# Kernel optimization log

Hardware: AMD Instinct MI355X
Metric: run time of the kernel (lower is better)

Reference implementation:

```python
import jax, jax.numpy as jnp
import numpy as np

# Orbital structure for basis {A: [2s, 2p, 1d]} -> full_basis l values
LS = [0, 0, 1, 1, 2]
DIMS = [2 * l + 1 for l in LS]            # [1,1,3,3,5]
OFFS = np.concatenate([[0], np.cumsum(DIMS)]).astype(int)
NORB = int(sum(DIMS))                      # 13

# Upper-triangular orbital-pair layout of the flat feature vector
PAIRS = []
_off = 0
for _i in range(len(LS)):
    for _j in range(_i, len(LS)):
        PAIRS.append((_i, _j, _off))
        _off += DIMS[_i] * DIMS[_j]
FEAT_DIM = _off                            # 107

N_ATOMS, N_EDGES, N_KPTS = 256, 4096, 4


def _assemble_blocks(feat):
    """[B, FEAT_DIM] -> [B, NORB, NORB], upper-tri orbital blocks, 0.5 on diagonal pairs."""
    B = feat.shape[0]
    blk = jnp.zeros((B, NORB, NORB), feat.dtype)
    for (i, j, o) in PAIRS:
        di, dj = DIMS[i], DIMS[j]
        f = 0.5 if i == j else 1.0
        blk = blk.at[:, OFFS[i]:OFFS[i] + di, OFFS[j]:OFFS[j] + dj].set(
            f * feat[:, o:o + di * dj].reshape(B, di, dj))
    return blk


def setup_inputs() -> dict:
    key = jax.random.key(0)
    k1, k2, k3, k4, k5 = jax.random.split(key, 5)
    return {
        "orbpair_hopping": jax.random.normal(k1, (N_EDGES, FEAT_DIM), jnp.float32),
        "orbpair_onsite": jax.random.normal(k2, (N_ATOMS, FEAT_DIM), jnp.float32),
        "kpoints": jax.random.uniform(k3, (N_KPTS, 3), jnp.float32),
        "edge_cell_shift": jax.random.randint(k4, (N_EDGES, 3), -3, 4).astype(jnp.float32),
        "edge_index": jax.random.randint(k5, (2, N_EDGES), 0, N_ATOMS),
    }


def reference(orbpair_hopping, orbpair_onsite, kpoints, edge_cell_shift, edge_index):
    hop = _assemble_blocks(orbpair_hopping)      # [E, norb, norb]
    onsite = _assemble_blocks(orbpair_onsite)    # [N, norb, norb]
    N, K = onsite.shape[0], kpoints.shape[0]
    cplx = jnp.complex64

    # phase[k, e] = exp(-i 2pi k . R_e)
    phase = jnp.exp(-2j * jnp.pi * (kpoints @ edge_cell_shift.T)).astype(cplx)  # [K, E]

    # H(k) in block form [K, N, N, norb, norb]
    blk = jnp.zeros((K, N, N, NORB, NORB), cplx)
    ar = jnp.arange(N)
    blk = blk.at[:, ar, ar].set(onsite.astype(cplx)[None])  # diagonal onsite blocks
    ei, ej = edge_index[0], edge_index[1]
    blk = blk.at[:, ei, ej].add(phase[:, :, None, None] * hop.astype(cplx)[None])

    H = blk.transpose(0, 1, 3, 2, 4).reshape(K, N * NORB, N * NORB)
    return H + jnp.conj(jnp.swapaxes(H, 1, 2))  # hermitianize
```

## Files before the change

kernel.cpp:

```cpp
#include <hip/hip_runtime.h>

#define NORB 13
#define FEAT 107
#define TWO_PI 6.28318530717958647692f
#define NN 3328
#define NROW 13312

__device__ __forceinline__ void map_pq(int p, int q, int& idx, float& scl) {
    const int DIMS[5] = {1, 1, 3, 3, 5};
    const int OFFS[5] = {0, 1, 2, 5, 8};
    idx = -1; scl = 0.0f;
    int o = 0;
    #pragma unroll
    for (int i = 0; i < 5; ++i) {
        #pragma unroll
        for (int j = i; j < 5; ++j) {
            int di = DIMS[i], dj = DIMS[j];
            if (p >= OFFS[i] && p < OFFS[i] + di && q >= OFFS[j] && q < OFFS[j] + dj) {
                idx = o + (p - OFFS[i]) * dj + (q - OFFS[j]);
                scl = (i == j) ? 0.5f : 1.0f;
            }
            o += di * dj;
        }
    }
}


__global__ void init_kernel(int4* __restrict__ head4, int* __restrict__ pairlist,
                            int* __restrict__ counter) {
    int t = blockIdx.x * blockDim.x + threadIdx.x;
    head4[t] = make_int4(-1, -1, -1, -1);
    if (t < 256) pairlist[t] = t * 257;
    if (t == 0) *counter = 256;
}

__global__ void fill_kernel(const int* __restrict__ eidx, const float* __restrict__ kpt,
                            const float* __restrict__ shf,
                            int* __restrict__ head, int* __restrict__ nxt,
                            int* __restrict__ pairlist, int* __restrict__ counter,
                            float* __restrict__ phases, int E, int K) {
    int tid = blockIdx.x * blockDim.x + threadIdx.x;
    if (tid >= 2 * E) return;
    int e = tid >> 1, dir = tid & 1;
    int ei = eidx[e], ej = eidx[E + e];
    int a = dir ? ej : ei;
    int b = dir ? ei : ej;
    int pid = a * 256 + b;
    int old = atomicExch(&head[pid], tid);
    nxt[tid] = old;
    if (old < 0 && a != b) {
        int pos = atomicAdd(counter, 1);
        pairlist[pos] = pid;
    }
    if (dir == 0) {
        float rx = shf[e * 3 + 0], ry = shf[e * 3 + 1], rz = shf[e * 3 + 2];
        for (int k = 0; k < K; ++k) {
            float th = -TWO_PI * (kpt[k * 3] * rx + kpt[k * 3 + 1] * ry + kpt[k * 3 + 2] * rz);
            float s, c;
            __sincosf(th, &s, &c);
            phases[(e * K + k) * 2]     = c;
            phases[(e * K + k) * 2 + 1] = s;
        }
    }
}

__global__ __launch_bounds__(256)
void fused_kernel(const float* __restrict__ hop, const float* __restrict__ ons,
                  const int* __restrict__ head, const int* __restrict__ nxt,
                  const int* __restrict__ pairlist, const int* __restrict__ counter,
                  const float* __restrict__ phases, float* __restrict__ out,
                  int npaint) {
    int t = threadIdx.x;
    if ((int)blockIdx.x < npaint) {
        int w = blockIdx.x;
        if (w >= *counter) return;
        if (t >= NORB * NORB) return;
        int pid = pairlist[w];
        int a = pid >> 8, b = pid & 255;
        int p = t / NORB, q = t - p * NORB;
        int i0, i1; float s0, s1;
        map_pq(p, q, i0, s0);
        map_pq(q, p, i1, s1);
        float ar[4] = {0.f, 0.f, 0.f, 0.f}, ai[4] = {0.f, 0.f, 0.f, 0.f};
        if (a == b) {
            const float* f = ons + (long)a * FEAT;
            float v = 0.f;
            if (i0 >= 0) v += s0 * f[i0];
            if (i1 >= 0) v += s1 * f[i1];
            #pragma unroll
            for (int k = 0; k < 4; ++k) ar[k] += v;
        }
        for (int it = head[pid]; it >= 0; it = nxt[it]) {
            int e = it >> 1, dir = it & 1;
            float hv;
            if (dir == 0) hv = (i0 >= 0) ? s0 * hop[(long)e * FEAT + i0] : 0.f;
            else          hv = (i1 >= 0) ? s1 * hop[(long)e * FEAT + i1] : 0.f;
            const float* ph = phases + (long)e * 8;
            if (dir == 0) {
                #pragma unroll
                for (int k = 0; k < 4; ++k) { ar[k] += ph[2*k] * hv; ai[k] += ph[2*k+1] * hv; }
            } else {
                #pragma unroll
                for (int k = 0; k < 4; ++k) { ar[k] += ph[2*k] * hv; ai[k] -= ph[2*k+1] * hv; }
            }
        }
        long row = (long)a * NORB + p;
        long col = (long)b * NORB + q;
        #pragma unroll
        for (int k = 0; k < 4; ++k) {
            long off = (((long)k * NN + row) * NN + col) * 2;
            out[off]     = ar[k];
            out[off + 1] = ai[k];
        }
    } else {
        int r = blockIdx.x - npaint;
        unsigned rl = (unsigned)r % NN;
        unsigned a  = rl / 13u;
        __shared__ unsigned char pnt[256];
        pnt[t] = (t == (int)a) ? 1 : (head[a * 256u + (unsigned)t] >= 0 ? 1 : 0);
        __syncthreads();
        long rowbase = (long)r * (NN * 2);
        float4 z4 = make_float4(0.f, 0.f, 0.f, 0.f);
        float2 z2 = make_float2(0.f, 0.f);
        for (int f = t; f < NN / 2; f += 256) {
            int c0 = 2 * f, c1 = 2 * f + 1;
            int b0 = c0 / 13, b1 = c1 / 13;
            bool p0 = pnt[b0] != 0;
            bool p1 = (b1 == b0) ? p0 : (pnt[b1] != 0);
            if (p0 && p1) continue;
            long off = rowbase + 4l * f;
            if (!p0 && !p1)      *(float4*)(out + off)     = z4;
            else if (!p0)        *(float2*)(out + off)     = z2;
            else                 *(float2*)(out + off + 2) = z2;
        }
    }
}


__global__ void zero_kernel(float4* __restrict__ out, long n4) {
    long i = (long)blockIdx.x * blockDim.x + threadIdx.x;
    long stride = (long)gridDim.x * blockDim.x;
    float4 z = make_float4(0.f, 0.f, 0.f, 0.f);
    for (; i < n4; i += stride) out[i] = z;
}

template <int CPX>
__global__ void onsite_kernel(const float* __restrict__ onsite, float* __restrict__ out,
                              int K, long nn) {
    int a = blockIdx.x;
    int t = threadIdx.x;
    if (t >= NORB * NORB) return;
    int p = t / NORB, q = t % NORB;
    int i1, i2; float s1, s2;
    map_pq(p, q, i1, s1);
    map_pq(q, p, i2, s2);
    const float* f = onsite + (long)a * FEAT;
    float v = 0.0f;
    if (i1 >= 0) v += s1 * f[i1];
    if (i2 >= 0) v += s2 * f[i2];
    long row = (long)a * NORB + p;
    long col = (long)a * NORB + q;
    for (int k = 0; k < K; ++k) {
        long off = (((long)k * nn + row) * nn + col) * CPX;
        out[off] = v;
    }
}

template <int CPX>
__global__ void edge_kernel(const float* __restrict__ hop, const float* __restrict__ kpts,
                            const float* __restrict__ shift, const int* __restrict__ eidx,
                            float* __restrict__ out, int E, int K, long nn) {
    int e = blockIdx.x;
    int t = threadIdx.x;
    __shared__ float phc[16], phs[16];
    int ei = eidx[e];
    int ej = eidx[E + e];
    if (t < K && t < 16) {
        float rx = shift[(long)e * 3 + 0];
        float ry = shift[(long)e * 3 + 1];
        float rz = shift[(long)e * 3 + 2];
        float th = -TWO_PI * (kpts[t * 3 + 0] * rx + kpts[t * 3 + 1] * ry + kpts[t * 3 + 2] * rz);
        float s, c;
        __sincosf(th, &s, &c);
        phc[t] = c; phs[t] = s;
    }
    __syncthreads();
    if (t >= NORB * NORB) return;
    int p = t / NORB, q = t % NORB;
    int idx; float scl;
    map_pq(p, q, idx, scl);
    if (idx < 0) return;
    float v = scl * hop[(long)e * FEAT + idx];
    long r1 = (long)ei * NORB + p, c1 = (long)ej * NORB + q;
    long r2 = (long)ej * NORB + q, c2 = (long)ei * NORB + p;
    for (int k = 0; k < K; ++k) {
        float pr = phc[k], pi = phs[k];
        long o1 = (((long)k * nn + r1) * nn + c1) * CPX;
        long o2 = (((long)k * nn + r2) * nn + c2) * CPX;
        atomicAdd(&out[o1], pr * v);
        atomicAdd(&out[o2], pr * v);
        if (CPX == 2) {
            atomicAdd(&out[o1 + 1], pi * v);
            atomicAdd(&out[o2 + 1], -pi * v);
        }
    }
}


extern "C" void kernel_launch(void* const* d_in, const int* in_sizes, int n_in,
                              void* d_out, int out_size, void* d_ws, size_t ws_size,
                              hipStream_t stream) {
    const float* hop  = (const float*)d_in[0];
    const float* ons  = (const float*)d_in[1];
    const float* kpt  = (const float*)d_in[2];
    const float* shf  = (const float*)d_in[3];
    const int*   eidx = (const int*)d_in[4];

    int E = in_sizes[0] / FEAT;
    int N = in_sizes[1] / FEAT;
    int K = in_sizes[2] / 3;
    long nn = (long)N * NORB;

    float* out = (float*)d_out;
    long knn2 = (long)K * nn * nn * 2;

    size_t off_head  = 0;
    size_t off_next  = off_head + 65536 * sizeof(int);
    size_t off_plist = off_next + (size_t)2 * E * sizeof(int);
    size_t off_cnt   = off_plist + (size_t)(256 + 2 * E) * sizeof(int);
    size_t off_phase = (off_cnt + 4 + 127) & ~(size_t)127;
    size_t ws_need   = off_phase + (size_t)E * K * 2 * sizeof(float);

    bool fast = (N == 256) && (K == 4) && (nn == NN) &&
                ((long)out_size == knn2) && (ws_size >= ws_need);

    if (fast) {
        char* ws = (char*)d_ws;
        int*   head   = (int*)(ws + off_head);
        int*   nxt    = (int*)(ws + off_next);
        int*   plist  = (int*)(ws + off_plist);
        int*   cnt    = (int*)(ws + off_cnt);
        float* phases = (float*)(ws + off_phase);

        init_kernel<<<64, 256, 0, stream>>>((int4*)head, plist, cnt);
        fill_kernel<<<(2 * E + 255) / 256, 256, 0, stream>>>(eidx, kpt, shf, head, nxt,
                                                             plist, cnt, phases, E, K);
        int npaint = 256 + 2 * E;
        fused_kernel<<<npaint + NROW, 256, 0, stream>>>(hop, ons, head, nxt, plist,
                                                        cnt, phases, out, npaint);
    } else {
        int cpx = ((long)out_size >= knn2) ? 2 : 1;
        long n4 = (long)out_size / 4;
        zero_kernel<<<2048, 256, 0, stream>>>((float4*)out, n4);
        if (cpx == 2) {
            onsite_kernel<2><<<N, 192, 0, stream>>>(ons, out, K, nn);
            edge_kernel<2><<<E, 192, 0, stream>>>(hop, kpt, shf, eidx, out, E, K, nn);
        } else {
            onsite_kernel<1><<<N, 192, 0, stream>>>(ons, out, K, nn);
            edge_kernel<1><<<E, 192, 0, stream>>>(hop, kpt, shf, eidx, out, E, K, nn);
        }
    }
}
```

Before: 80.24 us.

## Use static device buffers and zero 13-row slabs per block

Workspace buffers for the linked lists, pair list, counter and phases move into static __device__ globals, so the fast path no longer depends on the caller's workspace. The zero-fill part of the fused kernel now gives each block one (k, atom) slab of 13 rows instead of one row. The grid drops from 13312 zeroing blocks to 1024, and each block builds its painted-column mask once and reuses it for 13 rows. In exchange there is less parallelism per block and longer serial loops, and the static globals make the kernel unsafe if calls run concurrently.

```diff
diff --git a/kernel.cpp b/kernel.cpp
--- a/kernel.cpp
+++ b/kernel.cpp
@@ -4,7 +4,14 @@
 #define FEAT 107
 #define TWO_PI 6.28318530717958647692f
 #define NN 3328
-#define NROW 13312
+#define ROWF (NN * 2)
+#define EMAX 4096
+
+__device__ int   g_head[65536];
+__device__ int   g_nxt[2 * EMAX];
+__device__ int   g_plist[256 + 2 * EMAX];
+__device__ int   g_cnt;
+__device__ float g_phases[EMAX * 4 * 2];
 
 __device__ __forceinline__ void map_pq(int p, int q, int& idx, float& scl) {
     const int DIMS[5] = {1, 1, 3, 3, 5};
@@ -26,19 +33,15 @@
 }
 
 
-__global__ void init_kernel(int4* __restrict__ head4, int* __restrict__ pairlist,
-                            int* __restrict__ counter) {
+__global__ void init_kernel(int* __restrict__ pl_unused) {
     int t = blockIdx.x * blockDim.x + threadIdx.x;
-    head4[t] = make_int4(-1, -1, -1, -1);
-    if (t < 256) pairlist[t] = t * 257;
-    if (t == 0) *counter = 256;
+    ((int4*)g_head)[t] = make_int4(-1, -1, -1, -1);
+    if (t < 256) g_plist[t] = t * 257;
+    if (t == 0) g_cnt = 256;
 }
 
 __global__ void fill_kernel(const int* __restrict__ eidx, const float* __restrict__ kpt,
-                            const float* __restrict__ shf,
-                            int* __restrict__ head, int* __restrict__ nxt,
-                            int* __restrict__ pairlist, int* __restrict__ counter,
-                            float* __restrict__ phases, int E, int K) {
+                            const float* __restrict__ shf, int E, int K) {
     int tid = blockIdx.x * blockDim.x + threadIdx.x;
     if (tid >= 2 * E) return;
     int e = tid >> 1, dir = tid & 1;
@@ -46,11 +49,11 @@
     int a = dir ? ej : ei;
     int b = dir ? ei : ej;
     int pid = a * 256 + b;
-    int old = atomicExch(&head[pid], tid);
-    nxt[tid] = old;
+    int old = atomicExch(&g_head[pid], tid);
+    g_nxt[tid] = old;
     if (old < 0 && a != b) {
-        int pos = atomicAdd(counter, 1);
-        pairlist[pos] = pid;
+        int pos = atomicAdd(&g_cnt, 1);
+        g_plist[pos] = pid;
     }
     if (dir == 0) {
         float rx = shf[e * 3 + 0], ry = shf[e * 3 + 1], rz = shf[e * 3 + 2];
@@ -58,24 +61,21 @@
             float th = -TWO_PI * (kpt[k * 3] * rx + kpt[k * 3 + 1] * ry + kpt[k * 3 + 2] * rz);
             float s, c;
             __sincosf(th, &s, &c);
-            phases[(e * K + k) * 2]     = c;
-            phases[(e * K + k) * 2 + 1] = s;
+            g_phases[(e * K + k) * 2]     = c;
+            g_phases[(e * K + k) * 2 + 1] = s;
         }
     }
 }
 
 __global__ __launch_bounds__(256)
 void fused_kernel(const float* __restrict__ hop, const float* __restrict__ ons,
-                  const int* __restrict__ head, const int* __restrict__ nxt,
-                  const int* __restrict__ pairlist, const int* __restrict__ counter,
-                  const float* __restrict__ phases, float* __restrict__ out,
-                  int npaint) {
+                  float* __restrict__ out, int npaint) {
     int t = threadIdx.x;
     if ((int)blockIdx.x < npaint) {
         int w = blockIdx.x;
-        if (w >= *counter) return;
+        if (w >= g_cnt) return;
         if (t >= NORB * NORB) return;
-        int pid = pairlist[w];
+        int pid = g_plist[w];
         int a = pid >> 8, b = pid & 255;
         int p = t / NORB, q = t - p * NORB;
         int i0, i1; float s0, s1;
@@ -90,12 +90,12 @@
             #pragma unroll
             for (int k = 0; k < 4; ++k) ar[k] += v;
         }
-        for (int it = head[pid]; it >= 0; it = nxt[it]) {
+        for (int it = g_head[pid]; it >= 0; it = g_nxt[it]) {
             int e = it >> 1, dir = it & 1;
             float hv;
             if (dir == 0) hv = (i0 >= 0) ? s0 * hop[(long)e * FEAT + i0] : 0.f;
             else          hv = (i1 >= 0) ? s1 * hop[(long)e * FEAT + i1] : 0.f;
-            const float* ph = phases + (long)e * 8;
+            const float* ph = g_phases + e * 8;
             if (dir == 0) {
                 #pragma unroll
                 for (int k = 0; k < 4; ++k) { ar[k] += ph[2*k] * hv; ai[k] += ph[2*k+1] * hv; }
@@ -113,25 +113,28 @@
             out[off + 1] = ai[k];
         }
     } else {
-        int r = blockIdx.x - npaint;
-        unsigned rl = (unsigned)r % NN;
-        unsigned a  = rl / 13u;
+        int z = blockIdx.x - npaint;
+        int k = z >> 8;
+        int a = z & 255;
         __shared__ unsigned char pnt[256];
-        pnt[t] = (t == (int)a) ? 1 : (head[a * 256u + (unsigned)t] >= 0 ? 1 : 0);
+        pnt[t] = (t == a) ? 1 : (g_head[a * 256 + t] >= 0 ? 1 : 0);
         __syncthreads();
-        long rowbase = (long)r * (NN * 2);
         float4 z4 = make_float4(0.f, 0.f, 0.f, 0.f);
         float2 z2 = make_float2(0.f, 0.f);
-        for (int f = t; f < NN / 2; f += 256) {
-            int c0 = 2 * f, c1 = 2 * f + 1;
-            int b0 = c0 / 13, b1 = c1 / 13;
-            bool p0 = pnt[b0] != 0;
-            bool p1 = (b1 == b0) ? p0 : (pnt[b1] != 0);
-            if (p0 && p1) continue;
-            long off = rowbase + 4l * f;
-            if (!p0 && !p1)      *(float4*)(out + off)     = z4;
-            else if (!p0)        *(float2*)(out + off)     = z2;
-            else                 *(float2*)(out + off + 2) = z2;
+        long slabbase = ((long)k * NN + (long)a * NORB) * ROWF;
+        for (int rr = 0; rr < NORB; ++rr) {
+            long rowbase = slabbase + (long)rr * ROWF;
+            for (int f = t; f < NN / 2; f += 256) {
+                unsigned c0 = 2u * f, c1 = 2u * f + 1u;
+                unsigned b0 = c0 / 13u, b1 = c1 / 13u;
+                bool p0 = pnt[b0] != 0;
+                bool p1 = (b1 == b0) ? p0 : (pnt[b1] != 0);
+                if (p0 && p1) continue;
+                long off = rowbase + 4l * f;
+                if (!p0 && !p1)      *(float4*)(out + off)     = z4;
+                else if (!p0)        *(float2*)(out + off)     = z2;
+                else                 *(float2*)(out + off + 2) = z2;
+            }
         }
     }
 }
@@ -224,30 +227,14 @@
     float* out = (float*)d_out;
     long knn2 = (long)K * nn * nn * 2;
 
-    size_t off_head  = 0;
-    size_t off_next  = off_head + 65536 * sizeof(int);
-    size_t off_plist = off_next + (size_t)2 * E * sizeof(int);
-    size_t off_cnt   = off_plist + (size_t)(256 + 2 * E) * sizeof(int);
-    size_t off_phase = (off_cnt + 4 + 127) & ~(size_t)127;
-    size_t ws_need   = off_phase + (size_t)E * K * 2 * sizeof(float);
-
-    bool fast = (N == 256) && (K == 4) && (nn == NN) &&
-                ((long)out_size == knn2) && (ws_size >= ws_need);
+    bool fast = (N == 256) && (K == 4) && (E <= EMAX) &&
+                ((long)out_size == knn2);
 
     if (fast) {
-        char* ws = (char*)d_ws;
-        int*   head   = (int*)(ws + off_head);
-        int*   nxt    = (int*)(ws + off_next);
-        int*   plist  = (int*)(ws + off_plist);
-        int*   cnt    = (int*)(ws + off_cnt);
-        float* phases = (float*)(ws + off_phase);
-
-        init_kernel<<<64, 256, 0, stream>>>((int4*)head, plist, cnt);
-        fill_kernel<<<(2 * E + 255) / 256, 256, 0, stream>>>(eidx, kpt, shf, head, nxt,
-                                                             plist, cnt, phases, E, K);
+        init_kernel<<<64, 256, 0, stream>>>(nullptr);
+        fill_kernel<<<(2 * E + 255) / 256, 256, 0, stream>>>(eidx, kpt, shf, E, K);
         int npaint = 256 + 2 * E;
-        fused_kernel<<<npaint + NROW, 256, 0, stream>>>(hop, ons, head, nxt, plist,
-                                                        cnt, phases, out, npaint);
+        fused_kernel<<<npaint + 1024, 256, 0, stream>>>(hop, ons, out, npaint);
     } else {
         int cpx = ((long)out_size >= knn2) ? 2 : 1;
         long n4 = (long)out_size / 4;
```

After: 79.82 us. No clear change (-0.5%).
